# Optimization experiments

Hardware: AMD Instinct MI355X
Metric: run time of the kernel (lower is better)

The kernel has to match this reference:

```python
import jax, jax.numpy as jnp
from jax import lax
import numpy as np

EVAL_TERMS = 10   # eval mode: num_terms = eval_terms, update_iters = 0
INIT_ITERS = 50   # power iterations done in __init__
KSIZE = 3
IDX = np.array([0, 1, 1, 2, 3, 4, 2, 4, 3])  # maps 5 coeffs -> 3x3 kernel
EPS = 1e-12


def _l2n(t, axis):
    return t / (jnp.sqrt(jnp.sum(t * t, axis=axis, keepdims=True)) + EPS)


def setup_inputs() -> dict:
    key = jax.random.key(0)
    kx, kw, kb, ku, kv = jax.random.split(key, 5)
    C = 64
    stdv = 1.0 / np.sqrt(C)
    return {
        "x": jax.random.normal(kx, (16, C, 192, 192), dtype=jnp.float32),
        "random_conv_filter": jax.random.normal(kw, (C, C, 5), dtype=jnp.float32) * stdv,
        "bias": jax.random.uniform(kb, (C,), dtype=jnp.float32, minval=-stdv, maxval=stdv),
        "u0": jax.random.normal(ku, (5, 1, C), dtype=jnp.float32),
        "v0": jax.random.normal(kv, (5, C, 1), dtype=jnp.float32),
    }


def _power_iter(A, u0, v0):
    # A: (num, C, C) (stop-gradient), u: (num,1,C), v: (num,C,1)
    u = _l2n(u0, 2)
    v = _l2n(v0, 1)
    def body(i, uv):
        u, v = uv
        v = _l2n(jnp.sum(A * u, axis=2, keepdims=True), 1)
        u = _l2n(jnp.sum(A * v, axis=1, keepdims=True), 2)
        return (u, v)
    return lax.fori_loop(0, INIT_ITERS, body, (u, v))


def reference(x, random_conv_filter, bias, u0, v0):
    C = random_conv_filter.shape[0]
    # skew-symmetric filter per coefficient slice: A = 0.5*(W - W^T)
    A = 0.5 * (random_conv_filter - jnp.transpose(random_conv_filter, (1, 0, 2)))
    A = jnp.transpose(A, (2, 0, 1))  # (num, C, C)
    # spectral norm via power iteration (buffers; no grad)
    u, v = _power_iter(lax.stop_gradient(A), u0, v0)
    u = lax.stop_gradient(u)
    v = lax.stop_gradient(v)
    sigmas = jnp.sum(A * v * u, axis=(1, 2))  # (num,), grad flows through A only
    An = A / sigmas[:, None, None]
    # Taylor series of expm: I + An + An^2/2! + ... (eval_terms=10)
    curr = An
    Fm = An
    for i in range(2, EVAL_TERMS + 1):
        curr = jnp.einsum('nij,njk->nik', curr, An) / float(i)
        Fm = Fm + curr
    Fm = Fm + jnp.eye(C, dtype=Fm.dtype)[None]
    Fm = jnp.transpose(Fm, (1, 2, 0))  # (C, C, num)
    # expand 5 coeffs to 3x3 kernel, then spatial ifft2 -> real
    K = Fm[:, :, IDX].reshape(C, C, KSIZE, KSIZE)
    K = jnp.fft.ifft2(K, axes=(-2, -1)).real.astype(x.dtype)
    w = x.shape[2]
    pad = w // KSIZE  # circular pad and matching dilation
    xp = jnp.pad(x, ((0, 0), (0, 0), (pad, pad), (pad, pad)), mode='wrap')
    z = lax.conv_general_dilated(
        xp, K, window_strides=(1, 1), padding='VALID',
        rhs_dilation=(pad, pad),
        dimension_numbers=('NCHW', 'OIHW', 'NCHW'))
    return z + bias[None, :, None, None]
```

## Files before the change

### kernel.cpp

```cpp
#include <hip/hip_runtime.h>

typedef __attribute__((ext_vector_type(8))) short short8;
typedef __attribute__((ext_vector_type(4))) float f32x4;
typedef __attribute__((ext_vector_type(4))) float float4v;
typedef __attribute__((ext_vector_type(4))) unsigned int u32x4;

__device__ __forceinline__ unsigned short f2bf(float f) {
    unsigned int u = __float_as_uint(f);
    u += 0x7fffu + ((u >> 16) & 1u);
    return (unsigned short)(u >> 16);
}

__device__ __forceinline__ float wavesum(float x) {
#pragma unroll
    for (int m = 1; m < 64; m <<= 1) x += __shfl_xor(x, m);
    return x;
}

__device__ __forceinline__ float wavemax(float x) {
#pragma unroll
    for (int m = 1; m < 64; m <<= 1) x = fmaxf(x, __shfl_xor(x, m));
    return x;
}

__device__ __forceinline__ float matvec64(const float* row, float y) {
    float ac[8] = {0.f, 0.f, 0.f, 0.f, 0.f, 0.f, 0.f, 0.f};
#pragma unroll
    for (int j = 0; j < 64; ++j) {
        const float yj =
            __uint_as_float(__builtin_amdgcn_readlane(__float_as_uint(y), j));
        ac[j & 7] = fmaf(row[j], yj, ac[j & 7]);
    }
    return ((ac[0] + ac[1]) + (ac[2] + ac[3])) + ((ac[4] + ac[5]) + (ac[6] + ac[7]));
}

__device__ __forceinline__ void gload16(const void* g, void* l) {
    __builtin_amdgcn_global_load_lds(
        (const __attribute__((address_space(1))) unsigned int*)g,
        (__attribute__((address_space(3))) unsigned int*)l, 16, 0, 0);
}

#define WTF_OFF       81920
#define WTOLD_OFF     745472
#define XT_OFF        1441792
#define WS_NEEDED     76939264UL

#define FM_AFP   0
#define FM_R0    17408
#define FM_R1    34816
#define FM_SLOT  52224
#define FM_RED   76800
#define FM_SMEM  76928

__device__ __forceinline__ void fm_matmul_sb(char* sm, int srcOff, int bfSrcSlot,
                                             int dstOff, int bfDstSlot, int t) {
    const float* src = (const float*)(sm + srcOff);
    const unsigned short* bfS =
        (const unsigned short*)(sm + FM_SLOT) + bfSrcSlot * 4096;
    float* dst = (float*)(sm + dstOff);
    float* redf = (float*)(sm + FM_RED);
    const int lane = t & 63;
    const int wv = t >> 6;
    const int lm = lane & 15, lg = lane >> 4;
    f32x4 acc[4] = {};
    if (t < 256) {
#pragma unroll
        for (int kk = 0; kk < 2; ++kk) {
            const float* ap = src + (16 * wv + lm) * 68 + kk * 32 + lg * 8;
            const f32x4 a0 = *(const f32x4*)ap;
            const f32x4 a1 = *(const f32x4*)(ap + 4);
            short8 ah;
#pragma unroll
            for (int j = 0; j < 4; ++j) {
                ah[j] = (short)f2bf(a0[j]);
                ah[j + 4] = (short)f2bf(a1[j]);
            }
#pragma unroll
            for (int cf = 0; cf < 4; ++cf) {
                const short8 b =
                    *(const short8*)(bfS + ((kk * 4 + cf) * 64 + lane) * 8);
                acc[cf] = __builtin_amdgcn_mfma_f32_16x16x32_bf16(ah, b, acc[cf],
                                                                  0, 0, 0);
            }
        }
        float mx = 0.0f;
#pragma unroll
        for (int cf = 0; cf < 4; ++cf)
#pragma unroll
            for (int r = 0; r < 4; ++r) mx = fmaxf(mx, fabsf(acc[cf][r]));
        mx = wavemax(mx);
        if (lane == 0) redf[wv] = mx;
    }
    __syncthreads();
    if (t < 256) {
        const float g = fmaxf(fmaxf(redf[0], redf[1]), fmaxf(redf[2], redf[3]));
        const float sc = 1.0f / g;
        unsigned short* bfD = (unsigned short*)(sm + FM_SLOT) + bfDstSlot * 4096;
#pragma unroll
        for (int cf = 0; cf < 4; ++cf) {
#pragma unroll
            for (int r = 0; r < 4; ++r) {
                const int k = 16 * wv + 4 * lg + r;
                const int nn = 16 * cf + lm;
                const float v = acc[cf][r] * sc;
                dst[k * 68 + nn] = v;
                if (bfDstSlot >= 0)
                    bfD[(((k >> 5) * 4 + cf) * 64 + ((k & 31) >> 3) * 16 + lm) * 8 +
                        (k & 7)] = f2bf(v);
            }
        }
    }
    __syncthreads();
}

__global__ __launch_bounds__(512) void fmconv_kernel(const float* __restrict__ W,
                                                     const float* __restrict__ u0,
                                                     const float* __restrict__ x,
                                                     float* __restrict__ FmOut,
                                                     unsigned short* __restrict__ xT) {
    __shared__ __align__(16) char smem[FM_SMEM];
    const int t = threadIdx.x;

    if (blockIdx.x >= 5) {
        const int bb = blockIdx.x - 5;
        const int n = bb / 96;
        const int hpair = bb % 96;
        const int h = hpair * 2 + (t >> 8);
        const int tt = t & 255;
        const int w = tt >> 2;
        const int cg = tt & 3;
        const size_t xbase = ((size_t)(n * 64) * 192 + h) * 192;
        unsigned short* xTrow = xT + ((size_t)((n * 192 + h) * 2)) * 6144;

        float A0[8], A1[8];
#define CLOAD(S, R)                                                             \
    {                                                                           \
        const int half_ = (S) / 3, wb_ = (S) % 3;                               \
        _Pragma("unroll") for (int k = 0; k < 8; ++k)                           \
            R[k] = x[xbase + (size_t)(half_ * 32 + cg * 8 + k) * 36864 +        \
                     wb_ * 64 + w];                                             \
    }
#define CSTORE(S, R)                                                            \
    {                                                                           \
        const int half_ = (S) / 3, wb_ = (S) % 3;                               \
        union { unsigned short us[8]; short8 v; } pk;                           \
        _Pragma("unroll") for (int k = 0; k < 8; ++k) pk.us[k] = f2bf(R[k]);    \
        *(short8*)(xTrow + half_ * 6144 + (wb_ * 64 + w) * 32 + cg * 8) = pk.v; \
    }
        CLOAD(0, A0);
        CLOAD(1, A1);
        CSTORE(0, A0);
        CLOAD(2, A0);
        CSTORE(1, A1);
        CLOAD(3, A1);
        CSTORE(2, A0);
        CLOAD(4, A0);
        CSTORE(3, A1);
        CLOAD(5, A1);
        CSTORE(4, A0);
        CSTORE(5, A1);
#undef CLOAD
#undef CSTORE
        return;
    }

    float* Afp = (float*)(smem + FM_AFP);
    float* R0f = (float*)(smem + FM_R0);
    float* R1f = (float*)(smem + FM_R1);
    float* redf = (float*)(smem + FM_RED);
    float* sigP = redf + 4;
    const int n = blockIdx.x;
    const int lane = t & 63;
    const int wv = t >> 6;
    const int lm = lane & 15, lg = lane >> 4;

    {
        const int i = t >> 3;
        const int j0 = (t & 7) * 8;
#pragma unroll
        for (int k = 0; k < 8; ++k) {
            const int j = j0 + k;
            const float wij = W[(i * 64 + j) * 5 + n];
            const float wji = W[(j * 64 + i) * 5 + n];
            Afp[i * 68 + j] = 0.5f * (wij - wji);
        }
    }
    __syncthreads();

    if (t < 256) {
        unsigned short* s0 = (unsigned short*)(smem + FM_SLOT);
#pragma unroll
        for (int cf = 0; cf < 4; ++cf) {
#pragma unroll
            for (int r = 0; r < 4; ++r) {
                const int k = 16 * wv + 4 * lg + r;
                const int nn = 16 * cf + lm;
                s0[(((k >> 5) * 4 + cf) * 64 + ((k & 31) >> 3) * 16 + lm) * 8 +
                   (k & 7)] = f2bf(Afp[k * 68 + nn]);
            }
        }
    }
    __syncthreads();

    fm_matmul_sb(smem, FM_AFP, 0, FM_R0, 1, t);
    fm_matmul_sb(smem, FM_R0, 1, FM_R1, 2, t);
    fm_matmul_sb(smem, FM_R1, 2, FM_R0, 0, t);
    fm_matmul_sb(smem, FM_R0, 0, FM_R1, 2, t);
    fm_matmul_sb(smem, FM_R1, 2, FM_R0, 0, t);
    fm_matmul_sb(smem, FM_R0, 0, FM_R1, -1, t);
    fm_matmul_sb(smem, FM_R1, 0, FM_R0, -1, t);
    fm_matmul_sb(smem, FM_R0, 1, FM_R1, -1, t);

    if (t < 64) {
        float row[64];
#pragma unroll
        for (int q = 0; q < 16; ++q)
            *(f32x4*)&row[q * 4] = *(const f32x4*)&R1f[t * 68 + q * 4];
        float u = u0[n * 64 + t];
        u = u / (sqrtf(wavesum(u * u)) + 1e-12f);
        const float w = matvec64(row, u);
#pragma unroll
        for (int q = 0; q < 16; ++q)
            *(f32x4*)&row[q * 4] = *(const f32x4*)&Afp[t * 68 + q * 4];
        const float tt = matvec64(row, w);
        const float v = tt / (sqrtf(wavesum(tt * tt)) + 1e-12f);
        const float s = matvec64(row, v);
        const float u50 = -s / (sqrtf(wavesum(s * s)) + 1e-12f);
        const float t2 = matvec64(row, u50);
        const float sig = wavesum(v * t2);
        if (t == 0) *sigP = sig;
    }
    __syncthreads();

    const float inv_sig = 1.0f / (*sigP);
    float Fm[4][4];
    if (t < 256) {
        unsigned int* Anpk = (unsigned int*)(smem + FM_SLOT);
#pragma unroll
        for (int cf = 0; cf < 4; ++cf) {
#pragma unroll
            for (int r = 0; r < 4; ++r) {
                const int k = 16 * wv + 4 * lg + r;
                const int nn = 16 * cf + lm;
                const float v = Afp[k * 68 + nn] * inv_sig;
                R0f[k * 68 + nn] = v;
                const unsigned int ph = f2bf(v);
                const float hf = __uint_as_float(ph << 16);
                const unsigned int pl = f2bf(v - hf);
                Anpk[(((k >> 5) * 4 + cf) * 64 + ((k & 31) >> 3) * 16 + lm) * 8 +
                     (k & 7)] = ph | (pl << 16);
                Fm[cf][r] = v;
            }
        }
    }
    __syncthreads();

    for (int term = 2; term <= 10; ++term) {
        f32x4 acc[4] = {};
        if (t < 256) {
            const unsigned int* Anpk = (const unsigned int*)(smem + FM_SLOT);
#pragma unroll
            for (int kk = 0; kk < 2; ++kk) {
                const float* ap = R0f + (16 * wv + lm) * 68 + kk * 32 + lg * 8;
                const f32x4 a0 = *(const f32x4*)ap;
                const f32x4 a1 = *(const f32x4*)(ap + 4);
                short8 ah, al;
#pragma unroll
                for (int j = 0; j < 4; ++j) {
                    const unsigned int h0 = f2bf(a0[j]);
                    ah[j] = (short)h0;
                    al[j] = (short)f2bf(a0[j] - __uint_as_float(h0 << 16));
                    const unsigned int h1 = f2bf(a1[j]);
                    ah[j + 4] = (short)h1;
                    al[j + 4] = (short)f2bf(a1[j] - __uint_as_float(h1 << 16));
                }
#pragma unroll
                for (int cf = 0; cf < 4; ++cf) {
                    const unsigned int* pp = Anpk + ((kk * 4 + cf) * 64 + lane) * 8;
                    const u32x4 p0 = *(const u32x4*)pp;
                    const u32x4 p1 = *(const u32x4*)(pp + 4);
                    short8 bh, bl;
#pragma unroll
                    for (int j = 0; j < 4; ++j) {
                        bh[j] = (short)(p0[j] & 0xffffu);
                        bl[j] = (short)(p0[j] >> 16);
                        bh[j + 4] = (short)(p1[j] & 0xffffu);
                        bl[j + 4] = (short)(p1[j] >> 16);
                    }
                    acc[cf] = __builtin_amdgcn_mfma_f32_16x16x32_bf16(ah, bh,
                                                                      acc[cf], 0, 0, 0);
                    acc[cf] = __builtin_amdgcn_mfma_f32_16x16x32_bf16(ah, bl,
                                                                      acc[cf], 0, 0, 0);
                    acc[cf] = __builtin_amdgcn_mfma_f32_16x16x32_bf16(al, bh,
                                                                      acc[cf], 0, 0, 0);
                }
            }
        }
        __syncthreads();
        if (t < 256) {
            const float sc = 1.0f / (float)term;
#pragma unroll
            for (int cf = 0; cf < 4; ++cf) {
#pragma unroll
                for (int r = 0; r < 4; ++r) {
                    const int k = 16 * wv + 4 * lg + r;
                    const int nn = 16 * cf + lm;
                    const float v = acc[cf][r] * sc;
                    Fm[cf][r] += v;
                    if (term < 10) R0f[k * 68 + nn] = v;
                }
            }
        }
        __syncthreads();
    }

    if (t < 256) {
#pragma unroll
        for (int cf = 0; cf < 4; ++cf) {
#pragma unroll
            for (int r = 0; r < 4; ++r) {
                const int k = 16 * wv + 4 * lg + r;
                const int nn = 16 * cf + lm;
                FmOut[n * 4096 + k * 64 + nn] = Fm[cf][r] + ((k == nn) ? 1.0f : 0.0f);
            }
        }
    }
}

__global__ __launch_bounds__(256) void wbuild_kernel(const float* __restrict__ Fm,
                                                     unsigned short* __restrict__ Wtf,
                                                     unsigned short* __restrict__ WtOld) {
    const int tg = blockIdx.x * 256 + threadIdx.x;
    const int o = tg >> 6;
    const int i = tg & 63;
    float f[5];
#pragma unroll
    for (int nn = 0; nn < 5; ++nn) f[nn] = Fm[nn * 4096 + o * 64 + i];
    const int idx[3][3] = {{0, 1, 1}, {2, 3, 4}, {2, 4, 3}};
    float Kk[3][3];
#pragma unroll
    for (int u = 0; u < 3; ++u) {
#pragma unroll
        for (int v = 0; v < 3; ++v) {
            float s = 0.0f;
#pragma unroll
            for (int p = 0; p < 3; ++p) {
#pragma unroll
                for (int q = 0; q < 3; ++q) {
                    const int m = (p * u + q * v) % 3;
                    s += f[idx[p][q]] * ((m == 0) ? 1.0f : -0.5f);
                }
            }
            Kk[u][v] = s * (1.0f / 9.0f);
        }
    }
#pragma unroll
    for (int a = 0; a < 3; ++a) {
#pragma unroll
        for (int b = 0; b < 3; ++b) {
            const int m = (a * 3 + b) * 64 + o;
#pragma unroll
            for (int al = 0; al < 3; ++al) {
#pragma unroll
                for (int be = 0; be < 3; ++be) {
                    const int kh = (al - a + 4) % 3;
                    const int kw = (be - b + 4) % 3;
                    const unsigned short bf = f2bf(Kk[kh][kw]);
                    const int kap = (al * 3 + be) * 64 + i;
                    WtOld[m * 576 + kap] = bf;
                    const int MF = m >> 4, lmx = m & 15;
                    const int cc = kap >> 5, lgx = (kap >> 3) & 3, j = kap & 7;
                    Wtf[MF * 9216 + cc * 512 + (lgx * 16 + lmx) * 8 + j] = bf;
                }
            }
        }
    }
}

__global__ __launch_bounds__(256, 2) void gemm4_kernel(
    const unsigned short* __restrict__ xT, const unsigned short* __restrict__ Wtf,
    const float* __restrict__ bias, float* __restrict__ out) {
    __shared__ __align__(16) char smem[81920];
    const int t = threadIdx.x;
    const int lane = t & 63;
    const int wv = t >> 6;
    const int wm = wv >> 1;
    const int wp = wv & 1;
    const int lm = lane & 15;
    const int lg = lane >> 4;

    const int orig = blockIdx.x;
    const int swz = (orig & 7) * 192 + (orig >> 3);
    const int mg = swz % 3;
    const int panel = swz / 3;
    const int n = panel >> 5;
    const int h0b = (panel & 31) * 2;

    f32x4 acc[6][4] = {};

#define STAGE(BUF, KC)                                                          \
    {                                                                           \
        const int al_ = (KC) / 3, be_ = (KC) - 3 * ((KC) / 3);                  \
        _Pragma("unroll") for (int it = 0; it < 10; ++it) {                     \
            char* ldsb = smem + (BUF) * 40960 + it * 4096 + wv * 1024;          \
            const unsigned short* src;                                          \
            if (it < 6) {                                                       \
                const int e = it * 2048 + t * 8;                                \
                const int mfL = e >> 10;                                        \
                const int rem = e & 1023;                                       \
                src = Wtf + (mg * 12 + mfL) * 9216 + (KC) * 1024 + rem;         \
            } else {                                                            \
                const int e = (it - 6) * 2048 + t * 8;                          \
                const int ccL = e >> 12;                                        \
                const int rem = e & 4095;                                       \
                const int p_ = rem >> 5;                                        \
                const int c_ = rem & 31;                                        \
                const int h_ = h0b + (p_ >> 6) + 64 * al_;                      \
                const int w_ = be_ * 64 + (p_ & 63);                            \
                src = xT + ((size_t)((n * 192 + h_) * 2 + ccL)) * 6144 +        \
                      w_ * 32 + c_;                                             \
            }                                                                   \
            gload16(src, ldsb);                                                 \
        }                                                                       \
    }

#define COMPUTE(BUF)                                                            \
    {                                                                           \
        const char* base = smem + (BUF) * 40960;                                \
        short8 af[12];                                                          \
        short8 bf[8];                                                           \
        _Pragma("unroll") for (int mf = 0; mf < 6; ++mf)                        \
            _Pragma("unroll") for (int cl = 0; cl < 2; ++cl)                    \
                af[mf * 2 + cl] = *(const short8*)(                             \
                    base + (wm * 6 + mf) * 2048 + cl * 1024 + lane * 16);       \
        _Pragma("unroll") for (int pf = 0; pf < 4; ++pf)                        \
            _Pragma("unroll") for (int cl = 0; cl < 2; ++cl)                    \
                bf[pf * 2 + cl] = *(const short8*)(                             \
                    base + 24576 + cl * 8192 +                                  \
                    (wp * 64 + pf * 16 + lm) * 64 + lg * 16);                   \
        _Pragma("unroll") for (int cl = 0; cl < 2; ++cl)                        \
            _Pragma("unroll") for (int mf = 0; mf < 6; ++mf)                    \
                _Pragma("unroll") for (int pf = 0; pf < 4; ++pf)                \
                    acc[mf][pf] = __builtin_amdgcn_mfma_f32_16x16x32_bf16(      \
                        af[mf * 2 + cl], bf[pf * 2 + cl], acc[mf][pf], 0, 0, 0);\
    }

    STAGE(0, 0);
    __syncthreads();
#pragma unroll
    for (int kc = 0; kc < 9; ++kc) {
        const int b = kc & 1;
        if (kc < 8) STAGE(b ^ 1, kc + 1);
        COMPUTE(b);
        if (kc < 8) __syncthreads();
    }
#undef STAGE
#undef COMPUTE

    const int h0 = h0b + wp;
#pragma unroll
    for (int mf = 0; mf < 6; ++mf) {
#pragma unroll
        for (int r = 0; r < 4; ++r) {
            const int m = mg * 192 + wm * 96 + mf * 16 + lg * 4 + r;
            const int o = m & 63;
            const int ab2 = m >> 6;
            const float bo = bias[o];
            const int rowoff =
                ((n * 64 + o) * 192 + (h0 + 64 * (ab2 / 3))) * 192 + 64 * (ab2 % 3);
#pragma unroll
            for (int pf = 0; pf < 4; ++pf) {
                out[rowoff + pf * 16 + lm] = acc[mf][pf][r] + bo;
            }
        }
    }
}

__global__ __launch_bounds__(256) void gemm_fallback(const float* __restrict__ x,
                                                     const unsigned short* __restrict__ Wt,
                                                     const float* __restrict__ bias,
                                                     float* __restrict__ out) {
    __shared__ unsigned short Xs[64][36];
    const int t = threadIdx.x;
    const int lane = t & 63;
    const int wv = t >> 6;
    const int pblk = blockIdx.x;
    const int mg = blockIdx.y;
    const int n = pblk >> 6;
    const int h0 = pblk & 63;
    const int wave_m0 = mg * 192 + wv * 48;
    const int lm = lane & 15;
    const int lg = lane >> 4;

    f32x4 acc[3][4] = {};
    const float* xb = x + n * 64 * 36864;
    const int w0s = t & 63;
    const int kq = (t >> 6) * 8;

    for (int c = 0; c < 18; ++c) {
        const int ab = c >> 1;
        const int al = ab / 3;
        const int be = ab % 3;
        const int ih = (c & 1) * 32;
        const int base = ih * 36864 + (h0 + 64 * al) * 192 + 64 * be + w0s;
#pragma unroll
        for (int s = 0; s < 8; ++s) {
            const int kp = kq + s;
            Xs[w0s][kp] = f2bf(xb[base + kp * 36864]);
        }
        __syncthreads();
        const int kb = c * 32 + lg * 8;
        short8 af[3];
#pragma unroll
        for (int mf = 0; mf < 3; ++mf)
            af[mf] = *(const short8*)(Wt + (wave_m0 + mf * 16 + lm) * 576 + kb);
        short8 bf[4];
#pragma unroll
        for (int pf = 0; pf < 4; ++pf) {
            union { short8 v; unsigned long long q[2]; } u;
            const unsigned long long* s8 =
                (const unsigned long long*)(&Xs[pf * 16 + lm][lg * 8]);
            u.q[0] = s8[0];
            u.q[1] = s8[1];
            bf[pf] = u.v;
        }
#pragma unroll
        for (int mf = 0; mf < 3; ++mf)
#pragma unroll
            for (int pf = 0; pf < 4; ++pf)
                acc[mf][pf] = __builtin_amdgcn_mfma_f32_16x16x32_bf16(
                    af[mf], bf[pf], acc[mf][pf], 0, 0, 0);
        __syncthreads();
    }

#pragma unroll
    for (int mf = 0; mf < 3; ++mf)
#pragma unroll
        for (int r = 0; r < 4; ++r) {
            const int m = wave_m0 + mf * 16 + lg * 4 + r;
            const int o = m & 63;
            const int ab2 = m >> 6;
            const float bo = bias[o];
            const int rowoff =
                ((n * 64 + o) * 192 + (h0 + 64 * (ab2 / 3))) * 192 + 64 * (ab2 % 3);
#pragma unroll
            for (int pf = 0; pf < 4; ++pf)
                out[rowoff + pf * 16 + lm] = acc[mf][pf][r] + bo;
        }
}

extern "C" void kernel_launch(void* const* d_in, const int* in_sizes, int n_in,
                              void* d_out, int out_size, void* d_ws, size_t ws_size,
                              hipStream_t stream) {
    (void)in_sizes; (void)n_in; (void)out_size;
    const float* x = (const float*)d_in[0];
    const float* W = (const float*)d_in[1];
    const float* bias = (const float*)d_in[2];
    const float* u0 = (const float*)d_in[3];
    float* out = (float*)d_out;

    float* Fm = (float*)d_ws;
    unsigned short* Wtf = (unsigned short*)((char*)d_ws + WTF_OFF);
    unsigned short* WtOld = (unsigned short*)((char*)d_ws + WTOLD_OFF);
    unsigned short* xT = (unsigned short*)((char*)d_ws + XT_OFF);

    const bool big_ws = (ws_size >= WS_NEEDED);

    if (big_ws) {
        fmconv_kernel<<<5 + 1536, 512, 0, stream>>>(W, u0, x, Fm, xT);
        wbuild_kernel<<<16, 256, 0, stream>>>(Fm, Wtf, WtOld);
        gemm4_kernel<<<1536, 256, 0, stream>>>(xT, Wtf, bias, out);
    } else {
        fmconv_kernel<<<5, 512, 0, stream>>>(W, u0, x, Fm, xT);
        wbuild_kernel<<<16, 256, 0, stream>>>(Fm, Wtf, WtOld);
        dim3 g(1024, 3, 1);
        gemm_fallback<<<g, 256, 0, stream>>>(x, WtOld, bias, out);
    }
}
```

Before: 111.4 us.

## Run expm Taylor chain in a single wave without block barriers

The power-iteration and Taylor-series matmul stages in the five filter blocks now run on one 64-lane wave instead of four waves. Each lane computes all four 16-row tiles with 16 independent MFMA accumulators. This removes every __syncthreads and the cross-wave max reduction through shared memory. The running Fm sum moves from registers into shared memory. The trade-off is four times more MFMA work per wave, but with more instruction-level parallelism and no barrier latency on a serial, latency-bound chain.

```diff
diff --git a/kernel.cpp b/kernel.cpp
--- a/kernel.cpp
+++ b/kernel.cpp
@@ -49,68 +49,66 @@
 #define FM_R0    17408
 #define FM_R1    34816
 #define FM_SLOT  52224
-#define FM_RED   76800
 #define FM_SMEM  76928
 
-__device__ __forceinline__ void fm_matmul_sb(char* sm, int srcOff, int bfSrcSlot,
-                                             int dstOff, int bfDstSlot, int t) {
+#define BFIDX(K, CF, LM) \
+    (((((K) >> 5) * 4 + (CF)) * 64 + (((K) & 31) >> 3) * 16 + (LM)) * 8 + ((K) & 7))
+
+__device__ __forceinline__ void fm_matmul_sw(char* sm, int srcOff, int bfSrcSlot,
+                                             int dstOff, int bfDstSlot, int lane) {
     const float* src = (const float*)(sm + srcOff);
     const unsigned short* bfS =
         (const unsigned short*)(sm + FM_SLOT) + bfSrcSlot * 4096;
     float* dst = (float*)(sm + dstOff);
-    float* redf = (float*)(sm + FM_RED);
-    const int lane = t & 63;
-    const int wv = t >> 6;
     const int lm = lane & 15, lg = lane >> 4;
-    f32x4 acc[4] = {};
-    if (t < 256) {
-#pragma unroll
-        for (int kk = 0; kk < 2; ++kk) {
-            const float* ap = src + (16 * wv + lm) * 68 + kk * 32 + lg * 8;
+    f32x4 acc[4][4] = {};
+#pragma unroll
+    for (int kk = 0; kk < 2; ++kk) {
+        short8 ah[4];
+#pragma unroll
+        for (int mi = 0; mi < 4; ++mi) {
+            const float* ap = src + (mi * 16 + lm) * 68 + kk * 32 + lg * 8;
             const f32x4 a0 = *(const f32x4*)ap;
             const f32x4 a1 = *(const f32x4*)(ap + 4);
-            short8 ah;
 #pragma unroll
             for (int j = 0; j < 4; ++j) {
-                ah[j] = (short)f2bf(a0[j]);
-                ah[j + 4] = (short)f2bf(a1[j]);
-            }
-#pragma unroll
-            for (int cf = 0; cf < 4; ++cf) {
-                const short8 b =
-                    *(const short8*)(bfS + ((kk * 4 + cf) * 64 + lane) * 8);
-                acc[cf] = __builtin_amdgcn_mfma_f32_16x16x32_bf16(ah, b, acc[cf],
-                                                                  0, 0, 0);
-            }
-        }
-        float mx = 0.0f;
+                ah[mi][j] = (short)f2bf(a0[j]);
+                ah[mi][j + 4] = (short)f2bf(a1[j]);
+            }
+        }
+#pragma unroll
+        for (int cf = 0; cf < 4; ++cf) {
+            const short8 b = *(const short8*)(bfS + ((kk * 4 + cf) * 64 + lane) * 8);
+#pragma unroll
+            for (int mi = 0; mi < 4; ++mi)
+                acc[mi][cf] = __builtin_amdgcn_mfma_f32_16x16x32_bf16(
+                    ah[mi], b, acc[mi][cf], 0, 0, 0);
+        }
+    }
+    float mx = 0.0f;
+#pragma unroll
+    for (int mi = 0; mi < 4; ++mi)
 #pragma unroll
         for (int cf = 0; cf < 4; ++cf)
 #pragma unroll
-            for (int r = 0; r < 4; ++r) mx = fmaxf(mx, fabsf(acc[cf][r]));
-        mx = wavemax(mx);
-        if (lane == 0) redf[wv] = mx;
-    }
-    __syncthreads();
-    if (t < 256) {
-        const float g = fmaxf(fmaxf(redf[0], redf[1]), fmaxf(redf[2], redf[3]));
-        const float sc = 1.0f / g;
-        unsigned short* bfD = (unsigned short*)(sm + FM_SLOT) + bfDstSlot * 4096;
+            for (int r = 0; r < 4; ++r) mx = fmaxf(mx, fabsf(acc[mi][cf][r]));
+    mx = wavemax(mx);
+    const float sc = 1.0f / mx;
+    unsigned short* bfD = (unsigned short*)(sm + FM_SLOT) + bfDstSlot * 4096;
+#pragma unroll
+    for (int mi = 0; mi < 4; ++mi) {
 #pragma unroll
         for (int cf = 0; cf < 4; ++cf) {
 #pragma unroll
             for (int r = 0; r < 4; ++r) {
-                const int k = 16 * wv + 4 * lg + r;
-                const int nn = 16 * cf + lm;
-                const float v = acc[cf][r] * sc;
+                const int k = mi * 16 + lg * 4 + r;
+                const int nn = cf * 16 + lm;
+                const float v = acc[mi][cf][r] * sc;
                 dst[k * 68 + nn] = v;
-                if (bfDstSlot >= 0)
-                    bfD[(((k >> 5) * 4 + cf) * 64 + ((k & 31) >> 3) * 16 + lm) * 8 +
-                        (k & 7)] = f2bf(v);
-            }
-        }
-    }
-    __syncthreads();
+                if (bfDstSlot >= 0) bfD[BFIDX(k, cf, lm)] = f2bf(v);
+            }
+        }
+    }
 }
 
 __global__ __launch_bounds__(512) void fmconv_kernel(const float* __restrict__ W,
@@ -167,12 +165,7 @@
     float* Afp = (float*)(smem + FM_AFP);
     float* R0f = (float*)(smem + FM_R0);
     float* R1f = (float*)(smem + FM_R1);
-    float* redf = (float*)(smem + FM_RED);
-    float* sigP = redf + 4;
     const int n = blockIdx.x;
-    const int lane = t & 63;
-    const int wv = t >> 6;
-    const int lm = lane & 15, lg = lane >> 4;
 
     {
         const int i = t >> 3;
@@ -186,145 +179,144 @@
         }
     }
     __syncthreads();
-
-    if (t < 256) {
+    if (t >= 64) return;
+
+    const int lane = t;
+    const int lm = lane & 15, lg = lane >> 4;
+
+    {
         unsigned short* s0 = (unsigned short*)(smem + FM_SLOT);
 #pragma unroll
-        for (int cf = 0; cf < 4; ++cf) {
-#pragma unroll
-            for (int r = 0; r < 4; ++r) {
-                const int k = 16 * wv + 4 * lg + r;
-                const int nn = 16 * cf + lm;
-                s0[(((k >> 5) * 4 + cf) * 64 + ((k & 31) >> 3) * 16 + lm) * 8 +
-                   (k & 7)] = f2bf(Afp[k * 68 + nn]);
-            }
-        }
-    }
-    __syncthreads();
-
-    fm_matmul_sb(smem, FM_AFP, 0, FM_R0, 1, t);
-    fm_matmul_sb(smem, FM_R0, 1, FM_R1, 2, t);
-    fm_matmul_sb(smem, FM_R1, 2, FM_R0, 0, t);
-    fm_matmul_sb(smem, FM_R0, 0, FM_R1, 2, t);
-    fm_matmul_sb(smem, FM_R1, 2, FM_R0, 0, t);
-    fm_matmul_sb(smem, FM_R0, 0, FM_R1, -1, t);
-    fm_matmul_sb(smem, FM_R1, 0, FM_R0, -1, t);
-    fm_matmul_sb(smem, FM_R0, 1, FM_R1, -1, t);
-
-    if (t < 64) {
+        for (int mi = 0; mi < 4; ++mi)
+#pragma unroll
+            for (int cf = 0; cf < 4; ++cf)
+#pragma unroll
+                for (int r = 0; r < 4; ++r) {
+                    const int k = mi * 16 + lg * 4 + r;
+                    const int nn = cf * 16 + lm;
+                    s0[BFIDX(k, cf, lm)] = f2bf(Afp[k * 68 + nn]);
+                }
+    }
+
+    fm_matmul_sw(smem, FM_AFP, 0, FM_R0, 1, lane);
+    fm_matmul_sw(smem, FM_R0, 1, FM_R1, 2, lane);
+    fm_matmul_sw(smem, FM_R1, 2, FM_R0, 0, lane);
+    fm_matmul_sw(smem, FM_R0, 0, FM_R1, 2, lane);
+    fm_matmul_sw(smem, FM_R1, 2, FM_R0, 0, lane);
+    fm_matmul_sw(smem, FM_R0, 0, FM_R1, -1, lane);
+    fm_matmul_sw(smem, FM_R1, 0, FM_R0, -1, lane);
+    fm_matmul_sw(smem, FM_R0, 1, FM_R1, -1, lane);
+
+    float sig;
+    {
         float row[64];
 #pragma unroll
         for (int q = 0; q < 16; ++q)
-            *(f32x4*)&row[q * 4] = *(const f32x4*)&R1f[t * 68 + q * 4];
-        float u = u0[n * 64 + t];
+            *(f32x4*)&row[q * 4] = *(const f32x4*)&R1f[lane * 68 + q * 4];
+        float u = u0[n * 64 + lane];
         u = u / (sqrtf(wavesum(u * u)) + 1e-12f);
         const float w = matvec64(row, u);
 #pragma unroll
         for (int q = 0; q < 16; ++q)
-            *(f32x4*)&row[q * 4] = *(const f32x4*)&Afp[t * 68 + q * 4];
+            *(f32x4*)&row[q * 4] = *(const f32x4*)&Afp[lane * 68 + q * 4];
         const float tt = matvec64(row, w);
         const float v = tt / (sqrtf(wavesum(tt * tt)) + 1e-12f);
         const float s = matvec64(row, v);
         const float u50 = -s / (sqrtf(wavesum(s * s)) + 1e-12f);
         const float t2 = matvec64(row, u50);
-        const float sig = wavesum(v * t2);
-        if (t == 0) *sigP = sig;
-    }
-    __syncthreads();
-
-    const float inv_sig = 1.0f / (*sigP);
-    float Fm[4][4];
-    if (t < 256) {
-        unsigned int* Anpk = (unsigned int*)(smem + FM_SLOT);
-#pragma unroll
-        for (int cf = 0; cf < 4; ++cf) {
+        sig = wavesum(v * t2);
+    }
+    const float inv_sig = 1.0f / sig;
+
+    float* FmL = R1f;
+    unsigned int* Anpk = (unsigned int*)(smem + FM_SLOT);
+#pragma unroll
+    for (int mi = 0; mi < 4; ++mi)
+#pragma unroll
+        for (int cf = 0; cf < 4; ++cf)
 #pragma unroll
             for (int r = 0; r < 4; ++r) {
-                const int k = 16 * wv + 4 * lg + r;
-                const int nn = 16 * cf + lm;
+                const int k = mi * 16 + lg * 4 + r;
+                const int nn = cf * 16 + lm;
                 const float v = Afp[k * 68 + nn] * inv_sig;
                 R0f[k * 68 + nn] = v;
                 const unsigned int ph = f2bf(v);
                 const float hf = __uint_as_float(ph << 16);
                 const unsigned int pl = f2bf(v - hf);
-                Anpk[(((k >> 5) * 4 + cf) * 64 + ((k & 31) >> 3) * 16 + lm) * 8 +
-                     (k & 7)] = ph | (pl << 16);
-                Fm[cf][r] = v;
-            }
-        }
-    }
-    __syncthreads();
+                Anpk[BFIDX(k, cf, lm)] = ph | (pl << 16);
+                FmL[k * 68 + nn] = v;
+            }
 
     for (int term = 2; term <= 10; ++term) {
-        f32x4 acc[4] = {};
-        if (t < 256) {
-            const unsigned int* Anpk = (const unsigned int*)(smem + FM_SLOT);
-#pragma unroll
-            for (int kk = 0; kk < 2; ++kk) {
-                const float* ap = R0f + (16 * wv + lm) * 68 + kk * 32 + lg * 8;
+        f32x4 acc[4][4] = {};
+#pragma unroll
+        for (int kk = 0; kk < 2; ++kk) {
+            short8 ah[4], al[4];
+#pragma unroll
+            for (int mi = 0; mi < 4; ++mi) {
+                const float* ap = R0f + (mi * 16 + lm) * 68 + kk * 32 + lg * 8;
                 const f32x4 a0 = *(const f32x4*)ap;
                 const f32x4 a1 = *(const f32x4*)(ap + 4);
-                short8 ah, al;
 #pragma unroll
                 for (int j = 0; j < 4; ++j) {
                     const unsigned int h0 = f2bf(a0[j]);
-                    ah[j] = (short)h0;
-                    al[j] = (short)f2bf(a0[j] - __uint_as_float(h0 << 16));
+                    ah[mi][j] = (short)h0;
+                    al[mi][j] = (short)f2bf(a0[j] - __uint_as_float(h0 << 16));
                     const unsigned int h1 = f2bf(a1[j]);
-                    ah[j + 4] = (short)h1;
-                    al[j + 4] = (short)f2bf(a1[j] - __uint_as_float(h1 << 16));
-                }
-#pragma unroll
-                for (int cf = 0; cf < 4; ++cf) {
-                    const unsigned int* pp = Anpk + ((kk * 4 + cf) * 64 + lane) * 8;
-                    const u32x4 p0 = *(const u32x4*)pp;
-                    const u32x4 p1 = *(const u32x4*)(pp + 4);
-                    short8 bh, bl;
-#pragma unroll
-                    for (int j = 0; j < 4; ++j) {
-                        bh[j] = (short)(p0[j] & 0xffffu);
-                        bl[j] = (short)(p0[j] >> 16);
-                        bh[j + 4] = (short)(p1[j] & 0xffffu);
-                        bl[j + 4] = (short)(p1[j] >> 16);
-                    }
-                    acc[cf] = __builtin_amdgcn_mfma_f32_16x16x32_bf16(ah, bh,
-                                                                      acc[cf], 0, 0, 0);
-                    acc[cf] = __builtin_amdgcn_mfma_f32_16x16x32_bf16(ah, bl,
-                                                                      acc[cf], 0, 0, 0);
-                    acc[cf] = __builtin_amdgcn_mfma_f32_16x16x32_bf16(al, bh,
-                                                                      acc[cf], 0, 0, 0);
-                }
-            }
-        }
-        __syncthreads();
-        if (t < 256) {
-            const float sc = 1.0f / (float)term;
+                    ah[mi][j + 4] = (short)h1;
+                    al[mi][j + 4] = (short)f2bf(a1[j] - __uint_as_float(h1 << 16));
+                }
+            }
 #pragma unroll
             for (int cf = 0; cf < 4; ++cf) {
+                const unsigned int* pp = Anpk + ((kk * 4 + cf) * 64 + lane) * 8;
+                const u32x4 p0 = *(const u32x4*)pp;
+                const u32x4 p1 = *(const u32x4*)(pp + 4);
+                short8 bh, bl;
+#pragma unroll
+                for (int j = 0; j < 4; ++j) {
+                    bh[j] = (short)(p0[j] & 0xffffu);
+                    bl[j] = (short)(p0[j] >> 16);
+                    bh[j + 4] = (short)(p1[j] & 0xffffu);
+                    bl[j + 4] = (short)(p1[j] >> 16);
+                }
+#pragma unroll
+                for (int mi = 0; mi < 4; ++mi) {
+                    acc[mi][cf] = __builtin_amdgcn_mfma_f32_16x16x32_bf16(
+                        ah[mi], bh, acc[mi][cf], 0, 0, 0);
+                    acc[mi][cf] = __builtin_amdgcn_mfma_f32_16x16x32_bf16(
+                        ah[mi], bl, acc[mi][cf], 0, 0, 0);
+                    acc[mi][cf] = __builtin_amdgcn_mfma_f32_16x16x32_bf16(
+                        al[mi], bh, acc[mi][cf], 0, 0, 0);
+                }
+            }
+        }
+        const float sc = 1.0f / (float)term;
+#pragma unroll
+        for (int mi = 0; mi < 4; ++mi)
+#pragma unroll
+            for (int cf = 0; cf < 4; ++cf)
 #pragma unroll
                 for (int r = 0; r < 4; ++r) {
-                    const int k = 16 * wv + 4 * lg + r;
-                    const int nn = 16 * cf + lm;
-                    const float v = acc[cf][r] * sc;
-                    Fm[cf][r] += v;
+                    const int k = mi * 16 + lg * 4 + r;
+                    const int nn = cf * 16 + lm;
+                    const float v = acc[mi][cf][r] * sc;
+                    FmL[k * 68 + nn] += v;
                     if (term < 10) R0f[k * 68 + nn] = v;
                 }
-            }
-        }
-        __syncthreads();
-    }
-
-    if (t < 256) {
-#pragma unroll
-        for (int cf = 0; cf < 4; ++cf) {
+    }
+
+#pragma unroll
+    for (int mi = 0; mi < 4; ++mi)
+#pragma unroll
+        for (int cf = 0; cf < 4; ++cf)
 #pragma unroll
             for (int r = 0; r < 4; ++r) {
-                const int k = 16 * wv + 4 * lg + r;
-                const int nn = 16 * cf + lm;
-                FmOut[n * 4096 + k * 64 + nn] = Fm[cf][r] + ((k == nn) ? 1.0f : 0.0f);
-            }
-        }
-    }
+                const int k = mi * 16 + lg * 4 + r;
+                const int nn = cf * 16 + lm;
+                FmOut[n * 4096 + k * 64 + nn] =
+                    FmL[k * 68 + nn] + ((k == nn) ? 1.0f : 0.0f);
+            }
 }
 
 __global__ __launch_bounds__(256) void wbuild_kernel(const float* __restrict__ Fm,
```

Measured after the change: 210.4 us. 88.8% more time.

## Rework Fm power-chain matmuls to drop packed bf16 slots and extra barriers

Applied to the files above, without the earlier changes.

The small matrix-exponential prologue kernel no longer keeps pre-packed bf16 copies of the B operand in shared memory. Instead the B fragments are converted from fp32 on the fly, and scaling uses per-buffer max values. This removes one barrier per squaring matmul and per Taylor term, and uses ping-pong buffers for the Taylor terms. The power-iteration chain is also restructured to seven squarings plus extra matvecs. This cuts shared-memory footprint and synchronisation, at the cost of more strided LDS reads and more conversion work per matmul. It only affects the tiny Fm part, not the large convolution.

```diff
diff --git a/kernel.cpp b/kernel.cpp
--- a/kernel.cpp
+++ b/kernel.cpp
@@ -2,7 +2,6 @@
 
 typedef __attribute__((ext_vector_type(8))) short short8;
 typedef __attribute__((ext_vector_type(4))) float f32x4;
-typedef __attribute__((ext_vector_type(4))) float float4v;
 typedef __attribute__((ext_vector_type(4))) unsigned int u32x4;
 
 __device__ __forceinline__ unsigned short f2bf(float f) {
@@ -45,42 +44,44 @@
 #define XT_OFF        1441792
 #define WS_NEEDED     76939264UL
 
-#define FM_AFP   0
-#define FM_R0    17408
-#define FM_R1    34816
-#define FM_SLOT  52224
-#define FM_RED   76800
-#define FM_SMEM  76928
-
-__device__ __forceinline__ void fm_matmul_sb(char* sm, int srcOff, int bfSrcSlot,
-                                             int dstOff, int bfDstSlot, int t) {
-    const float* src = (const float*)(sm + srcOff);
-    const unsigned short* bfS =
-        (const unsigned short*)(sm + FM_SLOT) + bfSrcSlot * 4096;
-    float* dst = (float*)(sm + dstOff);
-    float* redf = (float*)(sm + FM_RED);
+#define FM_BUFB  17408
+#define FM_RED   52224
+#define FM_SMEM  52288
+
+__device__ __forceinline__ void fm_mm1(char* sm, int sA, int sB, int sD, int t) {
     const int lane = t & 63;
     const int wv = t >> 6;
     const int lm = lane & 15, lg = lane >> 4;
-    f32x4 acc[4] = {};
+    float* red = (float*)(sm + FM_RED);
     if (t < 256) {
+        const float* A = (const float*)(sm + sA * FM_BUFB);
+        const float* B = (const float*)(sm + sB * FM_BUFB);
+        float* D = (float*)(sm + sD * FM_BUFB);
+        const float scA = 1.0f / fmaxf(fmaxf(red[sA * 4 + 0], red[sA * 4 + 1]),
+                                       fmaxf(red[sA * 4 + 2], red[sA * 4 + 3]));
+        const float scB = 1.0f / fmaxf(fmaxf(red[sB * 4 + 0], red[sB * 4 + 1]),
+                                       fmaxf(red[sB * 4 + 2], red[sB * 4 + 3]));
+        f32x4 acc[4] = {};
 #pragma unroll
         for (int kk = 0; kk < 2; ++kk) {
-            const float* ap = src + (16 * wv + lm) * 68 + kk * 32 + lg * 8;
+            const float* ap = A + (16 * wv + lm) * 68 + kk * 32 + lg * 8;
             const f32x4 a0 = *(const f32x4*)ap;
             const f32x4 a1 = *(const f32x4*)(ap + 4);
             short8 ah;
 #pragma unroll
             for (int j = 0; j < 4; ++j) {
-                ah[j] = (short)f2bf(a0[j]);
-                ah[j + 4] = (short)f2bf(a1[j]);
+                ah[j] = (short)f2bf(a0[j] * scA);
+                ah[j + 4] = (short)f2bf(a1[j] * scA);
             }
 #pragma unroll
             for (int cf = 0; cf < 4; ++cf) {
-                const short8 b =
-                    *(const short8*)(bfS + ((kk * 4 + cf) * 64 + lane) * 8);
-                acc[cf] = __builtin_amdgcn_mfma_f32_16x16x32_bf16(ah, b, acc[cf],
-                                                                  0, 0, 0);
+                short8 b;
+#pragma unroll
+                for (int j = 0; j < 8; ++j)
+                    b[j] = (short)f2bf(
+                        B[(kk * 32 + lg * 8 + j) * 68 + cf * 16 + lm] * scB);
+                acc[cf] =
+                    __builtin_amdgcn_mfma_f32_16x16x32_bf16(ah, b, acc[cf], 0, 0, 0);
             }
         }
         float mx = 0.0f;
@@ -89,26 +90,12 @@
 #pragma unroll
             for (int r = 0; r < 4; ++r) mx = fmaxf(mx, fabsf(acc[cf][r]));
         mx = wavemax(mx);
-        if (lane == 0) redf[wv] = mx;
-    }
-    __syncthreads();
-    if (t < 256) {
-        const float g = fmaxf(fmaxf(redf[0], redf[1]), fmaxf(redf[2], redf[3]));
-        const float sc = 1.0f / g;
-        unsigned short* bfD = (unsigned short*)(sm + FM_SLOT) + bfDstSlot * 4096;
-#pragma unroll
-        for (int cf = 0; cf < 4; ++cf) {
-#pragma unroll
-            for (int r = 0; r < 4; ++r) {
-                const int k = 16 * wv + 4 * lg + r;
-                const int nn = 16 * cf + lm;
-                const float v = acc[cf][r] * sc;
-                dst[k * 68 + nn] = v;
-                if (bfDstSlot >= 0)
-                    bfD[(((k >> 5) * 4 + cf) * 64 + ((k & 31) >> 3) * 16 + lm) * 8 +
-                        (k & 7)] = f2bf(v);
-            }
-        }
+        if (lane == 0) red[sD * 4 + wv] = mx;
+#pragma unroll
+        for (int cf = 0; cf < 4; ++cf)
+#pragma unroll
+            for (int r = 0; r < 4; ++r)
+                D[(16 * wv + 4 * lg + r) * 68 + cf * 16 + lm] = acc[cf][r];
     }
     __syncthreads();
 }
@@ -164,11 +151,10 @@
         return;
     }
 
-    float* Afp = (float*)(smem + FM_AFP);
-    float* R0f = (float*)(smem + FM_R0);
-    float* R1f = (float*)(smem + FM_R1);
-    float* redf = (float*)(smem + FM_RED);
-    float* sigP = redf + 4;
+    float* B0 = (float*)smem;
+    float* B2f = (float*)(smem + 2 * FM_BUFB);
+    float* red = (float*)(smem + FM_RED);
+    float* sigP = red + 12;
     const int n = blockIdx.x;
     const int lane = t & 63;
     const int wv = t >> 6;
@@ -182,86 +168,73 @@
             const int j = j0 + k;
             const float wij = W[(i * 64 + j) * 5 + n];
             const float wji = W[(j * 64 + i) * 5 + n];
-            Afp[i * 68 + j] = 0.5f * (wij - wji);
-        }
+            B0[i * 68 + j] = 0.5f * (wij - wji);
+        }
+        if (t < 4) red[t] = 1.0f;
     }
     __syncthreads();
 
-    if (t < 256) {
-        unsigned short* s0 = (unsigned short*)(smem + FM_SLOT);
-#pragma unroll
-        for (int cf = 0; cf < 4; ++cf) {
-#pragma unroll
-            for (int r = 0; r < 4; ++r) {
-                const int k = 16 * wv + 4 * lg + r;
-                const int nn = 16 * cf + lm;
-                s0[(((k >> 5) * 4 + cf) * 64 + ((k & 31) >> 3) * 16 + lm) * 8 +
-                   (k & 7)] = f2bf(Afp[k * 68 + nn]);
-            }
-        }
-    }
-    __syncthreads();
-
-    fm_matmul_sb(smem, FM_AFP, 0, FM_R0, 1, t);
-    fm_matmul_sb(smem, FM_R0, 1, FM_R1, 2, t);
-    fm_matmul_sb(smem, FM_R1, 2, FM_R0, 0, t);
-    fm_matmul_sb(smem, FM_R0, 0, FM_R1, 2, t);
-    fm_matmul_sb(smem, FM_R1, 2, FM_R0, 0, t);
-    fm_matmul_sb(smem, FM_R0, 0, FM_R1, -1, t);
-    fm_matmul_sb(smem, FM_R1, 0, FM_R0, -1, t);
-    fm_matmul_sb(smem, FM_R0, 1, FM_R1, -1, t);
+    fm_mm1(smem, 0, 0, 1, t);
+    fm_mm1(smem, 1, 1, 2, t);
+    fm_mm1(smem, 2, 2, 1, t);
+    fm_mm1(smem, 1, 1, 2, t);
+    fm_mm1(smem, 2, 2, 1, t);
+    fm_mm1(smem, 1, 1, 2, t);
+    fm_mm1(smem, 2, 1, 2, t);
 
     if (t < 64) {
         float row[64];
 #pragma unroll
         for (int q = 0; q < 16; ++q)
-            *(f32x4*)&row[q * 4] = *(const f32x4*)&R1f[t * 68 + q * 4];
-        float u = u0[n * 64 + t];
+            *(f32x4*)&row[q * 4] = *(const f32x4*)&B0[lane * 68 + q * 4];
+        float u = u0[n * 64 + lane];
         u = u / (sqrtf(wavesum(u * u)) + 1e-12f);
-        const float w = matvec64(row, u);
+        const float wA = matvec64(row, u);
+        const float wB = matvec64(row, wA);
 #pragma unroll
         for (int q = 0; q < 16; ++q)
-            *(f32x4*)&row[q * 4] = *(const f32x4*)&Afp[t * 68 + q * 4];
-        const float tt = matvec64(row, w);
-        const float v = tt / (sqrtf(wavesum(tt * tt)) + 1e-12f);
+            *(f32x4*)&row[q * 4] = *(const f32x4*)&B2f[lane * 68 + q * 4];
+        const float w3 = matvec64(row, wB);
+#pragma unroll
+        for (int q = 0; q < 16; ++q)
+            *(f32x4*)&row[q * 4] = *(const f32x4*)&B0[lane * 68 + q * 4];
+        const float tt2 = matvec64(row, w3);
+        const float v = tt2 / (sqrtf(wavesum(tt2 * tt2)) + 1e-12f);
         const float s = matvec64(row, v);
         const float u50 = -s / (sqrtf(wavesum(s * s)) + 1e-12f);
-        const float t2 = matvec64(row, u50);
-        const float sig = wavesum(v * t2);
-        if (t == 0) *sigP = sig;
+        const float t2b = matvec64(row, u50);
+        const float sig = wavesum(v * t2b);
+        if (lane == 0) *sigP = sig;
     }
     __syncthreads();
 
     const float inv_sig = 1.0f / (*sigP);
     float Fm[4][4];
     if (t < 256) {
-        unsigned int* Anpk = (unsigned int*)(smem + FM_SLOT);
-#pragma unroll
-        for (int cf = 0; cf < 4; ++cf) {
+#pragma unroll
+        for (int cf = 0; cf < 4; ++cf)
 #pragma unroll
             for (int r = 0; r < 4; ++r) {
                 const int k = 16 * wv + 4 * lg + r;
-                const int nn = 16 * cf + lm;
-                const float v = Afp[k * 68 + nn] * inv_sig;
-                R0f[k * 68 + nn] = v;
-                const unsigned int ph = f2bf(v);
-                const float hf = __uint_as_float(ph << 16);
-                const unsigned int pl = f2bf(v - hf);
-                Anpk[(((k >> 5) * 4 + cf) * 64 + ((k & 31) >> 3) * 16 + lm) * 8 +
-                     (k & 7)] = ph | (pl << 16);
+                const int nn = cf * 16 + lm;
+                const float v = B0[k * 68 + nn] * inv_sig;
+                B0[k * 68 + nn] = v;
                 Fm[cf][r] = v;
             }
-        }
-    }
-    __syncthreads();
+    }
 
     for (int term = 2; term <= 10; ++term) {
-        f32x4 acc[4] = {};
+        __syncthreads();
         if (t < 256) {
-            const unsigned int* Anpk = (const unsigned int*)(smem + FM_SLOT);
+            const int si = (term == 2) ? 0 : ((term & 1) ? 1 : 2);
+            const int di = (term & 1) ? 2 : 1;
+            const float* CUR = (const float*)(smem + si * FM_BUFB);
+            float* DST = (float*)(smem + di * FM_BUFB);
+            const float* An = B0;
+            f32x4 acc[4] = {};
 #pragma unroll
             for (int kk = 0; kk < 2; ++kk) {
-                const float* ap = R0f + (16 * wv + lm) * 68 + kk * 32 + lg * 8;
+                const float* ap = CUR + (16 * wv + lm) * 68 + kk * 32 + lg * 8;
                 const f32x4 a0 = *(const f32x4*)ap;
                 const f32x4 a1 = *(const f32x4*)(ap + 4);
                 short8 ah, al;
@@ -276,16 +249,13 @@
                 }
 #pragma unroll
                 for (int cf = 0; cf < 4; ++cf) {
-                    const unsigned int* pp = Anpk + ((kk * 4 + cf) * 64 + lane) * 8;
-                    const u32x4 p0 = *(const u32x4*)pp;
-                    const u32x4 p1 = *(const u32x4*)(pp + 4);
                     short8 bh, bl;
 #pragma unroll
-                    for (int j = 0; j < 4; ++j) {
-                        bh[j] = (short)(p0[j] & 0xffffu);
-                        bl[j] = (short)(p0[j] >> 16);
-                        bh[j + 4] = (short)(p1[j] & 0xffffu);
-                        bl[j + 4] = (short)(p1[j] >> 16);
+                    for (int j = 0; j < 8; ++j) {
+                        const float v = An[(kk * 32 + lg * 8 + j) * 68 + cf * 16 + lm];
+                        const unsigned int ph = f2bf(v);
+                        bh[j] = (short)ph;
+                        bl[j] = (short)f2bf(v - __uint_as_float(ph << 16));
                     }
                     acc[cf] = __builtin_amdgcn_mfma_f32_16x16x32_bf16(ah, bh,
                                                                       acc[cf], 0, 0, 0);
@@ -295,35 +265,29 @@
                                                                       acc[cf], 0, 0, 0);
                 }
             }
-        }
-        __syncthreads();
-        if (t < 256) {
             const float sc = 1.0f / (float)term;
 #pragma unroll
-            for (int cf = 0; cf < 4; ++cf) {
+            for (int cf = 0; cf < 4; ++cf)
 #pragma unroll
                 for (int r = 0; r < 4; ++r) {
                     const int k = 16 * wv + 4 * lg + r;
-                    const int nn = 16 * cf + lm;
+                    const int nn = cf * 16 + lm;
                     const float v = acc[cf][r] * sc;
                     Fm[cf][r] += v;
-                    if (term < 10) R0f[k * 68 + nn] = v;
+                    if (term < 10) DST[k * 68 + nn] = v;
                 }
-            }
-        }
-        __syncthreads();
+        }
     }
 
     if (t < 256) {
 #pragma unroll
-        for (int cf = 0; cf < 4; ++cf) {
+        for (int cf = 0; cf < 4; ++cf)
 #pragma unroll
             for (int r = 0; r < 4; ++r) {
                 const int k = 16 * wv + 4 * lg + r;
-                const int nn = 16 * cf + lm;
+                const int nn = cf * 16 + lm;
                 FmOut[n * 4096 + k * 64 + nn] = Fm[cf][r] + ((k == nn) ? 1.0f : 0.0f);
             }
-        }
     }
 }
 
```

After: 111.9 us. No clear change (+0.4%).
